# Performance work log

Hardware: AMD Instinct MI355X
Metric: run time of the kernel (lower is better)

## Reference

```python
import jax, jax.numpy as jnp
import numpy as np

L = 2048      # max_length / encoder sequence length
E = 1024      # eo_hidden_size
H = 1024      # hidden_size
D = 512       # embed_size
V = 32000     # vocab_size
MV = 32768    # max_vocab_size


def setup_inputs() -> dict:
    key = jax.random.key(0)
    ks = jax.random.split(key, 20)
    s = 0.02
    return {
        "inp": jax.random.randint(ks[0], (1,), 0, V),
        "hidden": jax.random.normal(ks[1], (1, 1, H), jnp.float32),
        "encoder_outputs": jax.random.normal(ks[2], (L, E), jnp.float32),
        "input_seq": jax.random.randint(ks[3], (L,), 0, MV),
        "pre_prob": jax.random.randint(ks[4], (L,), 0, 2),
        "emb": jax.random.normal(ks[5], (V, D), jnp.float32) * s,
        "attn_W": jax.random.normal(ks[6], (L, H + D), jnp.float32) * s,
        "attn_b": jnp.zeros((L,), jnp.float32),
        "comb_W": jax.random.normal(ks[7], (H, E + D), jnp.float32) * s,
        "comb_b": jnp.zeros((H,), jnp.float32),
        "W_ih": jax.random.normal(ks[8], (3 * H, H + E), jnp.float32) * s,
        "W_hh": jax.random.normal(ks[9], (3 * H, H), jnp.float32) * s,
        "b_ih": jnp.zeros((3 * H,), jnp.float32),
        "b_hh": jnp.zeros((3 * H,), jnp.float32),
        "Wo_W": jax.random.normal(ks[10], (V, H), jnp.float32) * s,
        "Wo_b": jnp.zeros((V,), jnp.float32),
        "Wc_W": jax.random.normal(ks[11], (H, E), jnp.float32) * s,
        "Wc_b": jnp.zeros((H,), jnp.float32),
    }


def reference(inp, hidden, encoder_outputs, input_seq, pre_prob,
              emb, attn_W, attn_b, comb_W, comb_b,
              W_ih, W_hh, b_ih, b_hh, Wo_W, Wo_b, Wc_W, Wc_b):
    tok = inp[0]
    # --- copy-mechanism selective read (int path, matches torch .long() trunc) ---
    sel_w = (input_seq == tok).astype(jnp.int32) * pre_prob.astype(jnp.int32)  # [L]
    eo_int = jax.lax.stop_gradient(encoder_outputs).astype(jnp.int32)          # trunc toward 0
    sel_reading = (sel_w @ eo_int).astype(jnp.float32)                          # [E]
    # --- embedding (OOV -> UNK id 2); dropout is identity in eval ---
    embed_idx = jnp.where(tok >= V, 2, tok)
    embedded = emb[embed_idx]                                                   # [D]
    h = hidden[0, 0]                                                            # [H]
    # --- attention over encoder outputs ---
    attn_weights = jax.nn.softmax(attn_W @ jnp.concatenate([embedded, h]) + attn_b)  # [L]
    attn_applied = attn_weights @ encoder_outputs                               # [E]
    out = jax.nn.relu(comb_W @ jnp.concatenate([embedded, attn_applied]) + comb_b)   # [H]
    # --- single GRU step (torch gate order: r, z, n) ---
    x = jnp.concatenate([out, sel_reading])                                     # [H+E]
    gi = W_ih @ x + b_ih
    gh = W_hh @ h + b_hh
    r = jax.nn.sigmoid(gi[:H] + gh[:H])
    z = jax.nn.sigmoid(gi[H:2 * H] + gh[H:2 * H])
    n = jnp.tanh(gi[2 * H:] + r * gh[2 * H:])
    h_new = (1.0 - z) * n + z * h                                               # [H]
    # --- generate vs copy scores ---
    score_g = Wo_W @ h_new + Wo_b                                               # [V]
    score_c = jnp.tanh(encoder_outputs @ Wc_W.T + Wc_b) @ h_new                 # [L]
    score = jax.nn.softmax(jnp.concatenate([score_g, score_c]))                 # [V+L]
    prob_g, prob_c = score[:V], score[V:]
    # pad generate probs to MV and scatter-add copy probs (== mm with one-hot)
    out1 = jnp.zeros((MV,), score.dtype).at[:V].set(prob_g)
    out1 = out1.at[input_seq].add(prob_c)
    out1 = jnp.where(out1 == 0, 1e-9, out1)
    out1 = out1.at[2].set(1e-9)
    out1 = jnp.log(out1)
    return (out1[None, :], h_new[None, None, :], attn_weights[None, :], prob_c[None, :])
```

## Files before the change

kernel.cpp:

```cpp
#include <hip/hip_runtime.h>
#include <math.h>

#define LQ 2048
#define EQ 1024
#define HQ 1024
#define DQ 512
#define VQ 32000
#define MVQ 32768

#define OUT1_OFF 0
#define HNEW_OFF 32768
#define AW_OFF   33792
#define PC_OFF   35840

typedef __attribute__((ext_vector_type(8))) short short8_t;
typedef __attribute__((ext_vector_type(8))) unsigned short ushort8_t;
typedef __attribute__((ext_vector_type(4))) float floatx4;

__device__ inline float wred(float v) {
    v += __shfl_down(v, 32);
    v += __shfl_down(v, 16);
    v += __shfl_down(v, 8);
    v += __shfl_down(v, 4);
    v += __shfl_down(v, 2);
    v += __shfl_down(v, 1);
    return v;
}
__device__ inline float wred_max(float v) {
    v = fmaxf(v, __shfl_down(v, 32));
    v = fmaxf(v, __shfl_down(v, 16));
    v = fmaxf(v, __shfl_down(v, 8));
    v = fmaxf(v, __shfl_down(v, 4));
    v = fmaxf(v, __shfl_down(v, 2));
    v = fmaxf(v, __shfl_down(v, 1));
    return v;
}
__device__ inline float sigmoidf_(float x) { return 1.0f / (1.0f + expf(-x)); }
__device__ inline unsigned short f2bf(float x) {
    unsigned int u = __float_as_uint(x);
    unsigned int r = (u + 0x7fffu + ((u >> 16) & 1u)) >> 16;
    return (unsigned short)r;
}
__device__ inline float bf2f(unsigned short b) {
    return __uint_as_float(((unsigned int)b) << 16);
}
__device__ __forceinline__ void gload16(const unsigned short* g,
                                        unsigned short* l) {
    __builtin_amdgcn_global_load_lds(
        (const __attribute__((address_space(1))) unsigned int*)g,
        (__attribute__((address_space(3))) unsigned int*)l, 16, 0, 0);
}

__global__ __launch_bounds__(256) void k_prep(
    const float* __restrict__ enc, const float* __restrict__ Wc,
    const int* __restrict__ inp, const int* __restrict__ input_seq,
    const int* __restrict__ pre_prob,
    const float* __restrict__ attn_W, const float* __restrict__ attn_b,
    const float* __restrict__ emb, const float* __restrict__ hidden,
    unsigned short* __restrict__ Ah, unsigned short* __restrict__ Al,
    unsigned short* __restrict__ Bh, unsigned short* __restrict__ Bl,
    float* __restrict__ x2, float* __restrict__ logits, float* __restrict__ aa)
{
    __shared__ int s_cnt;
    __shared__ int s_list[LQ];
    const int tid = threadIdx.x;
    const int bx = blockIdx.x;
    if (bx < 512) {
        if (bx < 4) aa[bx * 256 + tid] = 0.0f;
        int warp = tid >> 6, lane = tid & 63;
        int r = bx * 4 + warp;
        int tok = inp[0];
        int ei = (tok >= VQ) ? 2 : tok;
        const float4* Wr = (const float4*)(attn_W + (size_t)r * 1536);
        const float4* e4 = (const float4*)(emb + (size_t)ei * DQ);
        const float4* h4 = (const float4*)hidden;
        float acc = 0.0f;
        #pragma unroll
        for (int i = 0; i < 6; ++i) {
            int idx = lane + i * 64;
            float4 x = (idx < 128) ? e4[idx] : h4[idx - 128];
            float4 w = Wr[idx];
            acc += w.x * x.x + w.y * x.y + w.z * x.z + w.w * x.w;
        }
        acc = wred(acc);
        if (lane == 0) logits[r] = acc + attn_b[r];
        return;
    }
    if (bx == 512) {
        if (tid == 0) s_cnt = 0;
        __syncthreads();
        int tok = inp[0];
        for (int l = tid; l < LQ; l += 256) {
            if (input_seq[l] == tok && pre_prob[l] != 0) {
                int p = atomicAdd(&s_cnt, 1);
                s_list[p] = l;
            }
        }
        __syncthreads();
        int nm = s_cnt;
        for (int e = tid; e < EQ; e += 256) {
            int acc = 0;
            for (int j = 0; j < nm; ++j)
                acc += (int)enc[(size_t)s_list[j] * EQ + e];
            x2[HQ + e] = (float)acc;
        }
        return;
    }
    size_t e0 = ((size_t)(bx - 513) * 256 + tid) * 8;
    const float* src;
    unsigned short *hdst, *ldst;
    size_t off;
    if (e0 < (size_t)LQ * EQ) { src = enc; hdst = Ah; ldst = Al; off = e0; }
    else { src = Wc; hdst = Bh; ldst = Bl; off = e0 - (size_t)LQ * EQ; }
    float4 v0 = *(const float4*)(src + off);
    float4 v1 = *(const float4*)(src + off + 4);
    float vv[8] = {v0.x, v0.y, v0.z, v0.w, v1.x, v1.y, v1.z, v1.w};
    ushort8_t H, L;
    #pragma unroll
    for (int k = 0; k < 8; ++k) {
        float x = vv[k];
        unsigned short hb = f2bf(x);
        H[k] = hb;
        L[k] = f2bf(x - bf2f(hb));
    }
    *(ushort8_t*)(hdst + off) = H;
    *(ushort8_t*)(ldst + off) = L;
}

__global__ __launch_bounds__(256, 2) void k_gemm_fused(
    const unsigned short* __restrict__ Ah, const unsigned short* __restrict__ Al,
    const unsigned short* __restrict__ Bh, const unsigned short* __restrict__ Bl,
    float* __restrict__ T, const float* __restrict__ Wc_b,
    const float* __restrict__ logits, const float* __restrict__ enc,
    float* __restrict__ aa, float* __restrict__ aw_out,
    const float* __restrict__ W_ih, const float* __restrict__ W_hh,
    const float* __restrict__ comb_W, const int* __restrict__ inp,
    const float* __restrict__ emb, const float* __restrict__ hidden,
    const float* __restrict__ x2,
    float* __restrict__ gi_sel, float* __restrict__ gh_pre,
    float* __restrict__ pre_c)
{
    __shared__ unsigned short sm[2 * 4 * 4096];
    const int b = blockIdx.x, t = threadIdx.x;
    const int lane = t & 63, wid = t >> 6;

    if (b < 512) {
        const int n0 = (b & 15) * 64;
        const int m0 = (b >> 4) * 64;
        const unsigned short* tsrc =
            (wid == 0) ? Ah + (size_t)m0 * EQ :
            (wid == 1) ? Al + (size_t)m0 * EQ :
            (wid == 2) ? Bh + (size_t)n0 * EQ :
                         Bl + (size_t)n0 * EQ;
        const int srow = lane >> 3;
        const int schunk = lane & 7;
        const int gch = schunk ^ srow;
        const int wm = (wid >> 1) * 32, wn = (wid & 1) * 32;
        const int fr = lane & 15, kg = lane >> 4;

        floatx4 acc[2][2];
        #pragma unroll
        for (int i = 0; i < 2; ++i)
            #pragma unroll
            for (int j = 0; j < 2; ++j)
                acc[i][j] = (floatx4){0.f, 0.f, 0.f, 0.f};

        #define STAGE(buf, s)                                                  \
            {                                                                  \
                unsigned short* dst = sm + (buf) * 16384 + wid * 4096;         \
                _Pragma("unroll")                                              \
                for (int c = 0; c < 8; ++c) {                                  \
                    int row = c * 8 + srow;                                    \
                    gload16(tsrc + (size_t)row * EQ + (s) * 64 + gch * 8,      \
                            dst + c * 512);                                    \
                }                                                              \
            }

        STAGE(0, 0);
        __syncthreads();
        for (int s = 0; s < 16; ++s) {
            int cur = s & 1;
            if (s < 15) STAGE(cur ^ 1, s + 1);
            const char* base = (const char*)sm + cur * 32768;
            #pragma unroll
            for (int kk = 0; kk < 2; ++kk) {
                short8_t fah[2], fal[2], fbh[2], fbl[2];
                #pragma unroll
                for (int f = 0; f < 2; ++f) {
                    int ra = wm + f * 16 + fr;
                    int oa = ra * 128 + (((kk * 4 + kg) ^ (ra & 7)) * 16);
                    fah[f] = *(const short8_t*)(base + oa);
                    fal[f] = *(const short8_t*)(base + 8192 + oa);
                    int rb = wn + f * 16 + fr;
                    int ob = rb * 128 + (((kk * 4 + kg) ^ (rb & 7)) * 16);
                    fbh[f] = *(const short8_t*)(base + 16384 + ob);
                    fbl[f] = *(const short8_t*)(base + 24576 + ob);
                }
                #pragma unroll
                for (int i = 0; i < 2; ++i)
                    #pragma unroll
                    for (int j = 0; j < 2; ++j) {
                        acc[i][j] = __builtin_amdgcn_mfma_f32_16x16x32_bf16(
                            fah[i], fbh[j], acc[i][j], 0, 0, 0);
                        acc[i][j] = __builtin_amdgcn_mfma_f32_16x16x32_bf16(
                            fal[i], fbh[j], acc[i][j], 0, 0, 0);
                        acc[i][j] = __builtin_amdgcn_mfma_f32_16x16x32_bf16(
                            fah[i], fbl[j], acc[i][j], 0, 0, 0);
                    }
            }
            __syncthreads();
        }
        #pragma unroll
        for (int i = 0; i < 2; ++i)
            #pragma unroll
            for (int j = 0; j < 2; ++j) {
                int row = m0 + wm + i * 16 + kg * 4;
                int col = n0 + wn + j * 16 + fr;
                float bj = Wc_b[col];
                #pragma unroll
                for (int r = 0; r < 4; ++r)
                    T[(size_t)(row + r) * HQ + col] = tanhf(acc[i][j][r] + bj);
            }
        return;
    }
    if (b < 576) {
        float* sred = (float*)sm;
        float* s_w  = (float*)sm + 8;
        int sb = b - 512;
        int xb = sb & 3, yb = sb >> 2;
        float m = -3.4e38f;
        for (int i = t; i < LQ; i += 256) m = fmaxf(m, logits[i]);
        m = wred_max(m);
        if (lane == 0) sred[wid] = m;
        __syncthreads();
        if (t == 0)
            sred[0] = fmaxf(fmaxf(sred[0], sred[1]), fmaxf(sred[2], sred[3]));
        __syncthreads();
        m = sred[0];
        __syncthreads();
        float s = 0.0f;
        for (int i = t; i < LQ; i += 256) s += expf(logits[i] - m);
        s = wred(s);
        if (lane == 0) sred[wid] = s;
        __syncthreads();
        if (t == 0) sred[0] = sred[0] + sred[1] + sred[2] + sred[3];
        __syncthreads();
        s = sred[0];
        int l0 = yb * 128;
        if (t < 128) {
            float w = expf(logits[l0 + t] - m) / s;
            s_w[t] = w;
            if (xb == 0) aw_out[l0 + t] = w;
        }
        __syncthreads();
        int e = xb * 256 + t;
        float acc = 0.0f;
        for (int l = 0; l < 128; ++l)
            acc = fmaf(s_w[l], enc[(size_t)(l0 + l) * EQ + e], acc);
        atomicAdd(&aa[e], acc);
        return;
    }
    if (b < 1344) {
        int row = (b - 576) * 4 + wid;
        const float4* Wr = (const float4*)(W_ih + (size_t)row * 2048 + 1024);
        const float4* xs = (const float4*)(x2 + HQ);
        float acc = 0.0f;
        #pragma unroll
        for (int c = 0; c < 4; ++c) {
            int idx = lane + c * 64;
            float4 w = Wr[idx], x = xs[idx];
            acc += w.x * x.x + w.y * x.y + w.z * x.z + w.w * x.w;
        }
        acc = wred(acc);
        if (lane == 0) gi_sel[row] = acc;
        return;
    }
    if (b < 2112) {
        int row = (b - 1344) * 4 + wid;
        const float4* Wr = (const float4*)(W_hh + (size_t)row * 1024);
        const float4* hv = (const float4*)hidden;
        float acc = 0.0f;
        #pragma unroll
        for (int c = 0; c < 4; ++c) {
            int idx = lane + c * 64;
            float4 w = Wr[idx], x = hv[idx];
            acc += w.x * x.x + w.y * x.y + w.z * x.z + w.w * x.w;
        }
        acc = wred(acc);
        if (lane == 0) gh_pre[row] = acc;
        return;
    }
    {
        int row = (b - 2112) * 4 + wid;
        int tok = inp[0];
        int ei = (tok >= VQ) ? 2 : tok;
        const float4* Wr = (const float4*)(comb_W + (size_t)row * 1536);
        const float4* e4 = (const float4*)(emb + (size_t)ei * DQ);
        float acc = 0.0f;
        #pragma unroll
        for (int c = 0; c < 2; ++c) {
            int idx = lane + c * 64;
            float4 w = Wr[idx], x = e4[idx];
            acc += w.x * x.x + w.y * x.y + w.z * x.z + w.w * x.w;
        }
        acc = wred(acc);
        if (lane == 0) pre_c[row] = acc;
        return;
    }
}

__global__ __launch_bounds__(256) void k_comb(
    const float* __restrict__ W, const float* __restrict__ b,
    const float* __restrict__ pre_c, const float* __restrict__ aa,
    float* __restrict__ x2)
{
    int warp = threadIdx.x >> 6, lane = threadIdx.x & 63;
    int r = blockIdx.x * 4 + warp;
    const float4* Wr = (const float4*)(W + (size_t)r * 1536 + 512);
    const float4* a4 = (const float4*)aa;
    float acc = 0.0f;
    #pragma unroll
    for (int i = 0; i < 4; ++i) {
        int idx = lane + i * 64;
        float4 w = Wr[idx], x = a4[idx];
        acc += w.x * x.x + w.y * x.y + w.z * x.z + w.w * x.w;
    }
    acc = wred(acc);
    if (lane == 0) x2[r] = fmaxf(acc + pre_c[r] + b[r], 0.0f);
}

__global__ __launch_bounds__(256) void k_gru(
    const float* __restrict__ W_ih, const float* __restrict__ gi_sel,
    const float* __restrict__ gh_pre,
    const float* __restrict__ b_ih, const float* __restrict__ b_hh,
    const float* __restrict__ x2, const float* __restrict__ h,
    float* __restrict__ hnew, float* __restrict__ out_h)
{
    int warp = threadIdx.x >> 6, lane = threadIdx.x & 63;
    int i = blockIdx.x * 4 + warp;
    const float4* xv = (const float4*)x2;
    const float4* Wr = (const float4*)(W_ih + (size_t)i * 2048);
    const float4* Wz = (const float4*)(W_ih + (size_t)(HQ + i) * 2048);
    const float4* Wn = (const float4*)(W_ih + (size_t)(2 * HQ + i) * 2048);
    float ar = 0, az = 0, an = 0;
    #pragma unroll
    for (int c = 0; c < 4; ++c) {
        int idx = lane + c * 64;
        float4 x = xv[idx];
        float4 w = Wr[idx]; ar += w.x*x.x + w.y*x.y + w.z*x.z + w.w*x.w;
        w = Wz[idx];        az += w.x*x.x + w.y*x.y + w.z*x.z + w.w*x.w;
        w = Wn[idx];        an += w.x*x.x + w.y*x.y + w.z*x.z + w.w*x.w;
    }
    ar = wred(ar); az = wred(az); an = wred(an);
    if (lane == 0) {
        float gir = ar + gi_sel[i] + b_ih[i];
        float giz = az + gi_sel[HQ + i] + b_ih[HQ + i];
        float gin = an + gi_sel[2 * HQ + i] + b_ih[2 * HQ + i];
        float ghr = gh_pre[i] + b_hh[i];
        float ghz = gh_pre[HQ + i] + b_hh[HQ + i];
        float ghn = gh_pre[2 * HQ + i] + b_hh[2 * HQ + i];
        float r = sigmoidf_(gir + ghr);
        float z = sigmoidf_(giz + ghz);
        float n = tanhf(gin + r * ghn);
        float hn = (1.0f - z) * n + z * h[i];
        hnew[i] = hn;
        out_h[i] = hn;
    }
}

__global__ __launch_bounds__(256) void k_scores(
    const float* __restrict__ Wo_W, const float* __restrict__ Wo_b,
    const float* __restrict__ T, const float* __restrict__ hnew,
    float* __restrict__ score)
{
    int warp = threadIdx.x >> 6, lane = threadIdx.x & 63;
    int r = blockIdx.x * 4 + warp;
    const float4* hv = (const float4*)hnew;
    const float* Wr = (r < VQ) ? Wo_W + (size_t)r * HQ
                               : T + (size_t)(r - VQ) * HQ;
    const float4* W4 = (const float4*)Wr;
    float acc = 0.0f;
    #pragma unroll
    for (int i = 0; i < 4; ++i) {
        int idx = lane + i * 64;
        float4 w = W4[idx], x = hv[idx];
        acc += w.x * x.x + w.y * x.y + w.z * x.z + w.w * x.w;
    }
    acc = wred(acc);
    if (lane == 0) score[r] = acc + ((r < VQ) ? Wo_b[r] : 0.0f);
}

__global__ __launch_bounds__(256) void k_final(
    const float* __restrict__ score, const int* __restrict__ input_seq,
    float* __restrict__ out1, float* __restrict__ out_pc)
{
    __shared__ float sred[4];
    __shared__ float bins[256];
    const int N = VQ + LQ;
    int tid = threadIdx.x, wid = tid >> 6, lane = tid & 63;
    float m = -3.4e38f;
    for (int i = tid; i < N; i += 256) m = fmaxf(m, score[i]);
    m = wred_max(m);
    if (lane == 0) sred[wid] = m;
    __syncthreads();
    if (tid == 0)
        sred[0] = fmaxf(fmaxf(sred[0], sred[1]), fmaxf(sred[2], sred[3]));
    __syncthreads();
    m = sred[0];
    __syncthreads();
    float s = 0.0f;
    for (int i = tid; i < N; i += 256) s += expf(score[i] - m);
    s = wred(s);
    if (lane == 0) sred[wid] = s;
    __syncthreads();
    if (tid == 0) sred[0] = sred[0] + sred[1] + sred[2] + sred[3];
    __syncthreads();
    s = sred[0];
    bins[tid] = 0.0f;
    __syncthreads();
    int i0 = blockIdx.x * 256;
    for (int l = tid; l < LQ; l += 256) {
        int si = input_seq[l];
        if (si >= i0 && si < i0 + 256)
            atomicAdd(&bins[si - i0], expf(score[VQ + l] - m) / s);
    }
    if (blockIdx.x < 8) {
        int l = blockIdx.x * 256 + tid;
        out_pc[l] = expf(score[VQ + l] - m) / s;
    }
    __syncthreads();
    int i = i0 + tid;
    float v = ((i < VQ) ? expf(score[i] - m) / s : 0.0f) + bins[tid];
    if (i == 2 || v == 0.0f) v = 1e-9f;
    out1[i] = logf(v);
}

extern "C" void kernel_launch(void* const* d_in, const int* in_sizes, int n_in,
                              void* d_out, int out_size, void* d_ws, size_t ws_size,
                              hipStream_t stream) {
    const int*   inp       = (const int*)  d_in[0];
    const float* hidden    = (const float*)d_in[1];
    const float* enc       = (const float*)d_in[2];
    const int*   input_seq = (const int*)  d_in[3];
    const int*   pre_prob  = (const int*)  d_in[4];
    const float* emb       = (const float*)d_in[5];
    const float* attn_W    = (const float*)d_in[6];
    const float* attn_b    = (const float*)d_in[7];
    const float* comb_W    = (const float*)d_in[8];
    const float* comb_b    = (const float*)d_in[9];
    const float* W_ih      = (const float*)d_in[10];
    const float* W_hh      = (const float*)d_in[11];
    const float* b_ih      = (const float*)d_in[12];
    const float* b_hh      = (const float*)d_in[13];
    const float* Wo_W      = (const float*)d_in[14];
    const float* Wo_b      = (const float*)d_in[15];
    const float* Wc_W      = (const float*)d_in[16];
    const float* Wc_b      = (const float*)d_in[17];

    float* out = (float*)d_out;

    unsigned short* Ah = (unsigned short*)d_ws;
    unsigned short* Al = Ah + (size_t)LQ * EQ;
    unsigned short* Bh = Al + (size_t)LQ * EQ;
    unsigned short* Bl = Bh + (size_t)HQ * EQ;
    float* T      = (float*)(Bl + (size_t)HQ * EQ);
    float* x2     = T + (size_t)LQ * HQ;
    float* hnew   = x2 + 2048;
    float* logits = hnew + 1024;
    float* aa     = logits + 2048;
    float* score  = aa + 1024;
    float* gi_sel = score + 34048;
    float* gh_pre = gi_sel + 3072;
    float* pre_c  = gh_pre + 3072;

    k_prep<<<2049, 256, 0, stream>>>(enc, Wc_W, inp, input_seq, pre_prob,
                                     attn_W, attn_b, emb, hidden,
                                     Ah, Al, Bh, Bl, x2, logits, aa);
    k_gemm_fused<<<2368, 256, 0, stream>>>(Ah, Al, Bh, Bl, T, Wc_b, logits,
                                           enc, aa, out + AW_OFF, W_ih, W_hh,
                                           comb_W, inp, emb, hidden, x2,
                                           gi_sel, gh_pre, pre_c);
    k_comb<<<HQ / 4, 256, 0, stream>>>(comb_W, comb_b, pre_c, aa, x2);
    k_gru<<<HQ / 4, 256, 0, stream>>>(W_ih, gi_sel, gh_pre, b_ih, b_hh, x2,
                                      hidden, hnew, out + HNEW_OFF);
    k_scores<<<(VQ + LQ) / 4, 256, 0, stream>>>(Wo_W, Wo_b, T, hnew, score);
    k_final<<<MVQ / 256, 256, 0, stream>>>(score, input_seq, out + OUT1_OFF,
                                           out + PC_OFF);
}
```

Baseline: 114.3 us.

## Enlarge GEMM tiles to 128x128 with XCD-aware mapping and batch GEMV rows per block

The split-bf16 GEMM for the copy-score projection now uses 128x128 output tiles with K=32 stages instead of 64x64 with K=64, so each wave holds a 4x4 grid of MFMA accumulators and reuses every loaded fragment across more MFMAs. The LDS swizzle is reworked for the new row stride. Block indices are mapped so that consecutive blocks landing on the same XCD share an M strip. The GEMV blocks in k_prep and k_gemm_fused now compute 16 rows per block instead of 4, which cuts the grid sizes. The trade-off is only 128 GEMM blocks (less parallelism across 256 CUs) and higher register pressure from 64 accumulator floats per lane.

```diff
diff --git a/kernel.cpp b/kernel.cpp
--- a/kernel.cpp
+++ b/kernel.cpp
@@ -65,28 +65,31 @@
     __shared__ int s_list[LQ];
     const int tid = threadIdx.x;
     const int bx = blockIdx.x;
-    if (bx < 512) {
+    if (bx < 128) {
         if (bx < 4) aa[bx * 256 + tid] = 0.0f;
         int warp = tid >> 6, lane = tid & 63;
-        int r = bx * 4 + warp;
         int tok = inp[0];
         int ei = (tok >= VQ) ? 2 : tok;
-        const float4* Wr = (const float4*)(attn_W + (size_t)r * 1536);
         const float4* e4 = (const float4*)(emb + (size_t)ei * DQ);
         const float4* h4 = (const float4*)hidden;
-        float acc = 0.0f;
-        #pragma unroll
-        for (int i = 0; i < 6; ++i) {
-            int idx = lane + i * 64;
-            float4 x = (idx < 128) ? e4[idx] : h4[idx - 128];
-            float4 w = Wr[idx];
-            acc += w.x * x.x + w.y * x.y + w.z * x.z + w.w * x.w;
-        }
-        acc = wred(acc);
-        if (lane == 0) logits[r] = acc + attn_b[r];
-        return;
-    }
-    if (bx == 512) {
+        #pragma unroll
+        for (int rr = 0; rr < 4; ++rr) {
+            int r = bx * 16 + warp * 4 + rr;
+            const float4* Wr = (const float4*)(attn_W + (size_t)r * 1536);
+            float acc = 0.0f;
+            #pragma unroll
+            for (int i = 0; i < 6; ++i) {
+                int idx = lane + i * 64;
+                float4 x = (idx < 128) ? e4[idx] : h4[idx - 128];
+                float4 w = Wr[idx];
+                acc += w.x * x.x + w.y * x.y + w.z * x.z + w.w * x.w;
+            }
+            acc = wred(acc);
+            if (lane == 0) logits[r] = acc + attn_b[r];
+        }
+        return;
+    }
+    if (bx == 128) {
         if (tid == 0) s_cnt = 0;
         __syncthreads();
         int tok = inp[0];
@@ -106,7 +109,7 @@
         }
         return;
     }
-    size_t e0 = ((size_t)(bx - 513) * 256 + tid) * 8;
+    size_t e0 = ((size_t)(bx - 129) * 256 + tid) * 8;
     const float* src;
     unsigned short *hdst, *ldst;
     size_t off;
@@ -144,25 +147,25 @@
     const int b = blockIdx.x, t = threadIdx.x;
     const int lane = t & 63, wid = t >> 6;
 
-    if (b < 512) {
-        const int n0 = (b & 15) * 64;
-        const int m0 = (b >> 4) * 64;
+    if (b < 128) {
+        const int xcd = b & 7, kk_ = b >> 3;
+        const int m0 = (xcd * 2 + (kk_ >> 3)) * 128;
+        const int n0 = (kk_ & 7) * 128;
         const unsigned short* tsrc =
             (wid == 0) ? Ah + (size_t)m0 * EQ :
             (wid == 1) ? Al + (size_t)m0 * EQ :
             (wid == 2) ? Bh + (size_t)n0 * EQ :
                          Bl + (size_t)n0 * EQ;
-        const int srow = lane >> 3;
-        const int schunk = lane & 7;
-        const int gch = schunk ^ srow;
-        const int wm = (wid >> 1) * 32, wn = (wid & 1) * 32;
+        const int srow = lane >> 2;
+        const int schunk = lane & 3;
+        const int wm = (wid >> 1) * 64, wn = (wid & 1) * 64;
         const int fr = lane & 15, kg = lane >> 4;
 
-        floatx4 acc[2][2];
-        #pragma unroll
-        for (int i = 0; i < 2; ++i)
-            #pragma unroll
-            for (int j = 0; j < 2; ++j)
+        floatx4 acc[4][4];
+        #pragma unroll
+        for (int i = 0; i < 4; ++i)
+            #pragma unroll
+            for (int j = 0; j < 4; ++j)
                 acc[i][j] = (floatx4){0.f, 0.f, 0.f, 0.f};
 
         #define STAGE(buf, s)                                                  \
@@ -170,50 +173,48 @@
                 unsigned short* dst = sm + (buf) * 16384 + wid * 4096;         \
                 _Pragma("unroll")                                              \
                 for (int c = 0; c < 8; ++c) {                                  \
-                    int row = c * 8 + srow;                                    \
-                    gload16(tsrc + (size_t)row * EQ + (s) * 64 + gch * 8,      \
+                    int row = c * 16 + srow;                                   \
+                    int gch = schunk ^ ((row >> 1) & 3);                       \
+                    gload16(tsrc + (size_t)row * EQ + (s) * 32 + gch * 8,      \
                             dst + c * 512);                                    \
                 }                                                              \
             }
 
         STAGE(0, 0);
         __syncthreads();
-        for (int s = 0; s < 16; ++s) {
+        for (int s = 0; s < 32; ++s) {
             int cur = s & 1;
-            if (s < 15) STAGE(cur ^ 1, s + 1);
+            if (s < 31) STAGE(cur ^ 1, s + 1);
             const char* base = (const char*)sm + cur * 32768;
-            #pragma unroll
-            for (int kk = 0; kk < 2; ++kk) {
-                short8_t fah[2], fal[2], fbh[2], fbl[2];
+            short8_t fah[4], fal[4], fbh[4], fbl[4];
+            #pragma unroll
+            for (int f = 0; f < 4; ++f) {
+                int ra = wm + f * 16 + fr;
+                int oa = ra * 64 + ((kg ^ ((ra >> 1) & 3)) * 16);
+                fah[f] = *(const short8_t*)(base + oa);
+                fal[f] = *(const short8_t*)(base + 8192 + oa);
+                int rb = wn + f * 16 + fr;
+                int ob = rb * 64 + ((kg ^ ((rb >> 1) & 3)) * 16);
+                fbh[f] = *(const short8_t*)(base + 16384 + ob);
+                fbl[f] = *(const short8_t*)(base + 24576 + ob);
+            }
+            #pragma unroll
+            for (int i = 0; i < 4; ++i)
                 #pragma unroll
-                for (int f = 0; f < 2; ++f) {
-                    int ra = wm + f * 16 + fr;
-                    int oa = ra * 128 + (((kk * 4 + kg) ^ (ra & 7)) * 16);
-                    fah[f] = *(const short8_t*)(base + oa);
-                    fal[f] = *(const short8_t*)(base + 8192 + oa);
-                    int rb = wn + f * 16 + fr;
-                    int ob = rb * 128 + (((kk * 4 + kg) ^ (rb & 7)) * 16);
-                    fbh[f] = *(const short8_t*)(base + 16384 + ob);
-                    fbl[f] = *(const short8_t*)(base + 24576 + ob);
+                for (int j = 0; j < 4; ++j) {
+                    acc[i][j] = __builtin_amdgcn_mfma_f32_16x16x32_bf16(
+                        fah[i], fbh[j], acc[i][j], 0, 0, 0);
+                    acc[i][j] = __builtin_amdgcn_mfma_f32_16x16x32_bf16(
+                        fal[i], fbh[j], acc[i][j], 0, 0, 0);
+                    acc[i][j] = __builtin_amdgcn_mfma_f32_16x16x32_bf16(
+                        fah[i], fbl[j], acc[i][j], 0, 0, 0);
                 }
-                #pragma unroll
-                for (int i = 0; i < 2; ++i)
-                    #pragma unroll
-                    for (int j = 0; j < 2; ++j) {
-                        acc[i][j] = __builtin_amdgcn_mfma_f32_16x16x32_bf16(
-                            fah[i], fbh[j], acc[i][j], 0, 0, 0);
-                        acc[i][j] = __builtin_amdgcn_mfma_f32_16x16x32_bf16(
-                            fal[i], fbh[j], acc[i][j], 0, 0, 0);
-                        acc[i][j] = __builtin_amdgcn_mfma_f32_16x16x32_bf16(
-                            fah[i], fbl[j], acc[i][j], 0, 0, 0);
-                    }
-            }
             __syncthreads();
         }
         #pragma unroll
-        for (int i = 0; i < 2; ++i)
-            #pragma unroll
-            for (int j = 0; j < 2; ++j) {
+        for (int i = 0; i < 4; ++i)
+            #pragma unroll
+            for (int j = 0; j < 4; ++j) {
                 int row = m0 + wm + i * 16 + kg * 4;
                 int col = n0 + wn + j * 16 + fr;
                 float bj = Wc_b[col];
@@ -223,10 +224,10 @@
             }
         return;
     }
-    if (b < 576) {
+    if (b < 192) {
         float* sred = (float*)sm;
         float* s_w  = (float*)sm + 8;
-        int sb = b - 512;
+        int sb = b - 128;
         int xb = sb & 3, yb = sb >> 2;
         float m = -3.4e38f;
         for (int i = t; i < LQ; i += 256) m = fmaxf(m, logits[i]);
@@ -260,51 +261,60 @@
         atomicAdd(&aa[e], acc);
         return;
     }
-    if (b < 1344) {
-        int row = (b - 576) * 4 + wid;
-        const float4* Wr = (const float4*)(W_ih + (size_t)row * 2048 + 1024);
+    if (b < 384) {
         const float4* xs = (const float4*)(x2 + HQ);
-        float acc = 0.0f;
-        #pragma unroll
-        for (int c = 0; c < 4; ++c) {
-            int idx = lane + c * 64;
-            float4 w = Wr[idx], x = xs[idx];
-            acc += w.x * x.x + w.y * x.y + w.z * x.z + w.w * x.w;
-        }
-        acc = wred(acc);
-        if (lane == 0) gi_sel[row] = acc;
-        return;
-    }
-    if (b < 2112) {
-        int row = (b - 1344) * 4 + wid;
-        const float4* Wr = (const float4*)(W_hh + (size_t)row * 1024);
+        #pragma unroll
+        for (int rr = 0; rr < 4; ++rr) {
+            int row = (b - 192) * 16 + wid * 4 + rr;
+            const float4* Wr = (const float4*)(W_ih + (size_t)row * 2048 + 1024);
+            float acc = 0.0f;
+            #pragma unroll
+            for (int c = 0; c < 4; ++c) {
+                int idx = lane + c * 64;
+                float4 w = Wr[idx], x = xs[idx];
+                acc += w.x * x.x + w.y * x.y + w.z * x.z + w.w * x.w;
+            }
+            acc = wred(acc);
+            if (lane == 0) gi_sel[row] = acc;
+        }
+        return;
+    }
+    if (b < 576) {
         const float4* hv = (const float4*)hidden;
-        float acc = 0.0f;
-        #pragma unroll
-        for (int c = 0; c < 4; ++c) {
-            int idx = lane + c * 64;
-            float4 w = Wr[idx], x = hv[idx];
-            acc += w.x * x.x + w.y * x.y + w.z * x.z + w.w * x.w;
-        }
-        acc = wred(acc);
-        if (lane == 0) gh_pre[row] = acc;
+        #pragma unroll
+        for (int rr = 0; rr < 4; ++rr) {
+            int row = (b - 384) * 16 + wid * 4 + rr;
+            const float4* Wr = (const float4*)(W_hh + (size_t)row * 1024);
+            float acc = 0.0f;
+            #pragma unroll
+            for (int c = 0; c < 4; ++c) {
+                int idx = lane + c * 64;
+                float4 w = Wr[idx], x = hv[idx];
+                acc += w.x * x.x + w.y * x.y + w.z * x.z + w.w * x.w;
+            }
+            acc = wred(acc);
+            if (lane == 0) gh_pre[row] = acc;
+        }
         return;
     }
     {
-        int row = (b - 2112) * 4 + wid;
         int tok = inp[0];
         int ei = (tok >= VQ) ? 2 : tok;
-        const float4* Wr = (const float4*)(comb_W + (size_t)row * 1536);
         const float4* e4 = (const float4*)(emb + (size_t)ei * DQ);
-        float acc = 0.0f;
-        #pragma unroll
-        for (int c = 0; c < 2; ++c) {
-            int idx = lane + c * 64;
-            float4 w = Wr[idx], x = e4[idx];
-            acc += w.x * x.x + w.y * x.y + w.z * x.z + w.w * x.w;
-        }
-        acc = wred(acc);
-        if (lane == 0) pre_c[row] = acc;
+        #pragma unroll
+        for (int rr = 0; rr < 4; ++rr) {
+            int row = (b - 576) * 16 + wid * 4 + rr;
+            const float4* Wr = (const float4*)(comb_W + (size_t)row * 1536);
+            float acc = 0.0f;
+            #pragma unroll
+            for (int c = 0; c < 2; ++c) {
+                int idx = lane + c * 64;
+                float4 w = Wr[idx], x = e4[idx];
+                acc += w.x * x.x + w.y * x.y + w.z * x.z + w.w * x.w;
+            }
+            acc = wred(acc);
+            if (lane == 0) pre_c[row] = acc;
+        }
         return;
     }
 }
@@ -473,13 +483,13 @@
     float* gh_pre = gi_sel + 3072;
     float* pre_c  = gh_pre + 3072;
 
-    k_prep<<<2049, 256, 0, stream>>>(enc, Wc_W, inp, input_seq, pre_prob,
+    k_prep<<<1665, 256, 0, stream>>>(enc, Wc_W, inp, input_seq, pre_prob,
                                      attn_W, attn_b, emb, hidden,
                                      Ah, Al, Bh, Bl, x2, logits, aa);
-    k_gemm_fused<<<2368, 256, 0, stream>>>(Ah, Al, Bh, Bl, T, Wc_b, logits,
-                                           enc, aa, out + AW_OFF, W_ih, W_hh,
-                                           comb_W, inp, emb, hidden, x2,
-                                           gi_sel, gh_pre, pre_c);
+    k_gemm_fused<<<640, 256, 0, stream>>>(Ah, Al, Bh, Bl, T, Wc_b, logits,
+                                          enc, aa, out + AW_OFF, W_ih, W_hh,
+                                          comb_W, inp, emb, hidden, x2,
+                                          gi_sel, gh_pre, pre_c);
     k_comb<<<HQ / 4, 256, 0, stream>>>(comb_W, comb_b, pre_c, aa, x2);
     k_gru<<<HQ / 4, 256, 0, stream>>>(W_ih, gi_sel, gh_pre, b_ih, b_hh, x2,
                                       hidden, hnew, out + HNEW_OFF);
```

Result: slower. 123.2 us (+7.8%).
